# Optimization experiments

Measured on AMD Instinct MI355X. Metric: run time of the kernel, lower is better.

## Reference

```python
import jax, jax.numpy as jnp
import numpy as np

B, I, H = 16384, 1024, 1024
W_SCALE = 0.03  # keep gate pre-activations in a sane range (mimics small init)


def setup_inputs() -> dict:
    key = jax.random.key(0)
    ks = jax.random.split(key, 7)
    return {
        "x": jax.random.normal(ks[0], (B, I), dtype=jnp.float32),
        "c": jax.random.normal(ks[1], (B, H), dtype=jnp.float32),
        "h": jax.random.normal(ks[2], (B, H), dtype=jnp.float32),
        # gate order along axis 0: f (forget), i (input), k (cell cand), o (output)
        "Wx": jax.random.normal(ks[3], (4, H, I), dtype=jnp.float32) * W_SCALE,
        "bx": jax.random.normal(ks[4], (4, H), dtype=jnp.float32) * W_SCALE,
        "Wh": jax.random.normal(ks[5], (4, H, H), dtype=jnp.float32) * W_SCALE,
        "bh": jax.random.normal(ks[6], (4, H), dtype=jnp.float32) * W_SCALE,
    }


def reference(x, c, h, Wx, bx, Wh, bh):
    # Fused equivalent of the 8 tiny nn.Linear calls: one stacked GEMM each
    # for input->hidden and hidden->hidden. pre: [B, 4, H]
    pre = (jnp.einsum('bi,ghi->bgh', x, Wx)
           + jnp.einsum('bk,ghk->bgh', h, Wh)
           + bx[None] + bh[None])
    f = jax.nn.sigmoid(pre[:, 0])   # forget gate (w1/r1)
    i = jax.nn.sigmoid(pre[:, 1])   # input gate  (w2/r2)
    k = jnp.tanh(pre[:, 2])         # cell candidate (w3/r3)
    o = jax.nn.sigmoid(pre[:, 3])   # output gate (w4/r4)
    c_new = f * c + i * k
    h_new = o * jnp.tanh(c_new)
    return (o, c_new, h_new)
```

## Files before the change

kernel.cpp:

```cpp
#include <hip/hip_runtime.h>
#include <hip/hip_bf16.h>
#include <cstdint>

#define DI __device__ __forceinline__

typedef __attribute__((ext_vector_type(4)))  float f32x4;
typedef __attribute__((ext_vector_type(16))) float f32x16;
typedef __attribute__((ext_vector_type(8)))  short bf16x8;

static constexpr int B_ = 16384, I_ = 1024, H_ = 1024;
static constexpr int M = B_;
static constexpr int N = 4 * H_;
static constexpr int K = I_ + H_;
static constexpr int NT = K / 64;

static constexpr size_t OFF_A  = 0;
static constexpr size_t OFF_W  = OFF_A + (size_t)M * K * 2;
static constexpr size_t OFF_BI = OFF_W + (size_t)N * K * 2;

DI unsigned short f2bf(float f) {
    union { float f; unsigned u; } v; v.f = f;
    unsigned r = v.u + 0x7FFFu + ((v.u >> 16) & 1u);
    return (unsigned short)(r >> 16);
}

__global__ void cvt_kernel(const float* __restrict__ x, const float* __restrict__ h,
                           const float* __restrict__ Wx, const float* __restrict__ Wh,
                           unsigned short* __restrict__ A, unsigned short* __restrict__ W)
{
    long tid = (long)blockIdx.x * blockDim.x + threadIdx.x;
    long row = tid >> 9;
    int  col = (int)(tid & 511) * 4;
    const float* src;
    unsigned short* dst;
    if (row < M) {
        src = (col < I_) ? x + (size_t)row * I_ + col
                         : h + (size_t)row * H_ + (col - I_);
        dst = A + (size_t)row * K + col;
    } else {
        int r = (int)(row - M);
        int gate = (r >> 5) & 3;
        int hcol = ((r >> 7) << 5) | (r & 31);
        int srow = gate * H_ + hcol;
        src = (col < I_) ? Wx + (size_t)srow * I_ + col
                         : Wh + (size_t)srow * H_ + (col - I_);
        dst = W + (size_t)r * K + col;
    }
    float4 v = *(const float4*)src;
    ushort4 o;
    o.x = f2bf(v.x); o.y = f2bf(v.y); o.z = f2bf(v.z); o.w = f2bf(v.w);
    *(ushort4*)dst = o;
}

__global__ void bias_kernel(const float* __restrict__ bx, const float* __restrict__ bh,
                            float* __restrict__ bias)
{
    int r = blockIdx.x * blockDim.x + threadIdx.x;
    if (r < N) {
        int gate = (r >> 5) & 3;
        int hcol = ((r >> 7) << 5) | (r & 31);
        int s = gate * H_ + hcol;
        bias[r] = bx[s] + bh[s];
    }
}

DI void stage_half(const unsigned short* __restrict__ g, int grow0, int kcol,
                   unsigned short* ldsbase, int tid)
{
    const int w    = tid >> 6, lane = tid & 63;
    const int rsub = (w << 3) + (lane >> 3);
    const int kk   = kcol + (((lane & 7) ^ (lane >> 3)) << 3);
#pragma unroll
    for (int l = 0; l < 2; ++l) {
        const unsigned short* gp = g + (size_t)(grow0 + (l << 6) + rsub) * K + kk;
        unsigned short* lp = ldsbase + (((l << 6) + (w << 3)) << 6);
        __builtin_amdgcn_global_load_lds(
            (const __attribute__((address_space(1))) void*)gp,
            (__attribute__((address_space(3))) void*)lp, 16, 0, 0);
    }
}

DI bf16x8 ldfrag32(const unsigned short* tile, int row, int s16, int lane)
{
    const int sl = (((s16 << 1) + (lane >> 5)) ^ (row & 7));
    return *(const bf16x8*)(tile + (row << 6) + (sl << 3));
}

DI float sigf(float v) { return 1.f / (1.f + __expf(-v)); }
DI float tanhfast(float v) {
    float vc = fminf(fmaxf(v, -15.f), 15.f);
    float e  = __expf(2.f * vc);
    return (e - 1.f) / (e + 1.f);
}

__global__ __launch_bounds__(512, 2) void gemm_lstm(
    const unsigned short* __restrict__ Abf, const unsigned short* __restrict__ Wbf,
    const float* __restrict__ bias, const float* __restrict__ c,
    float* __restrict__ out)
{
    __shared__ __align__(16) unsigned short sh[65536];

    const int tid  = threadIdx.x;
    const int lane = tid & 63;
    const int wid  = tid >> 6;
    const int wr   = wid >> 1;
    const int wc   = wid & 1;

    const int bid  = blockIdx.x;
    const int xcd  = bid & 7;
    const int loc  = bid >> 3;
    const int nbk  = (xcd << 1) | (loc & 1);
    const int mbk  = loc >> 1;
    const int brow = mbk << 8, bcol = nbk << 8;

    const int l31  = lane & 31;
    const int rA0  = (wr << 6) + l31;
    const int rB0  = (wc << 7) + l31;

    f32x16 acc[2][4];
#pragma unroll
    for (int i = 0; i < 2; ++i)
#pragma unroll
        for (int j = 0; j < 4; ++j)
#pragma unroll
            for (int e = 0; e < 16; ++e) acc[i][j][e] = 0.f;
    bf16x8 a[4], b[4][4];

    {
        stage_half(Abf, brow,       0, sh,         tid);
        stage_half(Abf, brow + 128, 0, sh + 8192,  tid);
        stage_half(Wbf, bcol,       0, sh + 16384, tid);
        stage_half(Wbf, bcol + 128, 0, sh + 24576, tid);
        asm volatile("s_waitcnt vmcnt(0)" ::: "memory");
        __builtin_amdgcn_s_barrier();
    }

    for (int t = 0; t < NT; ++t) {
        const int q = t & 1;
        unsigned short* curA = sh + q * 32768;
        unsigned short* curB = curA + 16384;
        unsigned short* nxtA = sh + (q ^ 1) * 32768;
        unsigned short* nxtB = nxtA + 16384;
        const int k1 = ((t + 1) & 31) << 6;

        stage_half(Abf, brow,       k1, nxtA,        tid);
        stage_half(Abf, brow + 128, k1, nxtA + 8192, tid);
        stage_half(Wbf, bcol,       k1, nxtB,        tid);
        stage_half(Wbf, bcol + 128, k1, nxtB + 8192, tid);

#pragma unroll
        for (int nt = 0; nt < 4; ++nt)
#pragma unroll
            for (int s = 0; s < 4; ++s)
                b[nt][s] = ldfrag32(curB, rB0 + nt * 32, s, lane);

#pragma unroll
        for (int s = 0; s < 4; ++s) a[s] = ldfrag32(curA, rA0, s, lane);
#pragma unroll
        for (int s = 0; s < 4; ++s)
#pragma unroll
            for (int nt = 0; nt < 4; ++nt)
                acc[0][nt] = __builtin_amdgcn_mfma_f32_32x32x16_bf16(
                    a[s], b[nt][s], acc[0][nt], 0, 0, 0);

#pragma unroll
        for (int s = 0; s < 4; ++s) a[s] = ldfrag32(curA, rA0 + 32, s, lane);
#pragma unroll
        for (int s = 0; s < 4; ++s)
#pragma unroll
            for (int nt = 0; nt < 4; ++nt)
                acc[1][nt] = __builtin_amdgcn_mfma_f32_32x32x16_bf16(
                    a[s], b[nt][s], acc[1][nt], 0, 0, 0);

        asm volatile("s_waitcnt vmcnt(0)" ::: "memory");
        __builtin_amdgcn_s_barrier();
    }

    const int c0    = bcol + (wc << 7);
    const int hcol  = ((c0 >> 7) << 5) + l31;
    const float bs0 = bias[c0 +       l31];
    const float bs1 = bias[c0 +  32 + l31];
    const float bs2 = bias[c0 +  64 + l31];
    const float bs3 = bias[c0 +  96 + l31];
    const int rbase = brow + (wr << 6) + ((lane >> 5) << 2);
    const size_t P  = (size_t)B_ * H_;
#pragma unroll
    for (int mt = 0; mt < 2; ++mt) {
#pragma unroll
        for (int r = 0; r < 16; ++r) {
            const int row = rbase + mt * 32 + (r & 3) + ((r >> 2) << 3);
            const size_t base = (size_t)row * H_ + hcol;
            float fg = sigf(acc[mt][0][r] + bs0);
            float ig = sigf(acc[mt][1][r] + bs1);
            float kg = tanhfast(acc[mt][2][r] + bs2);
            float og = sigf(acc[mt][3][r] + bs3);
            float cv = c[base];
            float cn = fg * cv + ig * kg;
            float hn = og * tanhfast(cn);
            out[base]         = og;
            out[P + base]     = cn;
            out[2 * P + base] = hn;
        }
    }
}

extern "C" void kernel_launch(void* const* d_in, const int* in_sizes, int n_in,
                              void* d_out, int out_size, void* d_ws, size_t ws_size,
                              hipStream_t stream)
{
    const float* x  = (const float*)d_in[0];
    const float* c  = (const float*)d_in[1];
    const float* h  = (const float*)d_in[2];
    const float* Wx = (const float*)d_in[3];
    const float* bx = (const float*)d_in[4];
    const float* Wh = (const float*)d_in[5];
    const float* bh = (const float*)d_in[6];

    unsigned short* Abf  = (unsigned short*)((char*)d_ws + OFF_A);
    unsigned short* Wbf  = (unsigned short*)((char*)d_ws + OFF_W);
    float*          bias = (float*)((char*)d_ws + OFF_BI);
    float*          out  = (float*)d_out;

    cvt_kernel<<<40960, 256, 0, stream>>>(x, h, Wx, Wh, Abf, Wbf);
    bias_kernel<<<16, 256, 0, stream>>>(bx, bh, bias);
    gemm_lstm<<<(M / 256) * (N / 256), 512, 0, stream>>>(
        Abf, Wbf, bias, c, out);
}
```

Before: 350.6 us.

## Stage GEMM tiles in fragment-major LDS layout for conflict-free MFMA loads

Replaces the row-major, XOR-swizzled LDS tile layout with a fragment-major layout. Each wave loads 32 rows times 16 k-elements per global_load_lds, so every MFMA operand fragment sits contiguously in LDS and is read with a plain lane-indexed 16-byte load, with no swizzle arithmetic. It also loads both A fragments up front and interleaves the MFMAs across both M tiles, which raises register use. The intent is to cut LDS bank conflicts and address math in the inner loop. The cost is global loads where each lane fetches only 16 bytes from a different row, which may coalesce worse.

```diff
diff --git a/kernel.cpp b/kernel.cpp
--- a/kernel.cpp
+++ b/kernel.cpp
@@ -4,7 +4,6 @@
 
 #define DI __device__ __forceinline__
 
-typedef __attribute__((ext_vector_type(4)))  float f32x4;
 typedef __attribute__((ext_vector_type(16))) float f32x16;
 typedef __attribute__((ext_vector_type(8)))  short bf16x8;
 
@@ -64,26 +63,12 @@
     }
 }
 
-DI void stage_half(const unsigned short* __restrict__ g, int grow0, int kcol,
-                   unsigned short* ldsbase, int tid)
-{
-    const int w    = tid >> 6, lane = tid & 63;
-    const int rsub = (w << 3) + (lane >> 3);
-    const int kk   = kcol + (((lane & 7) ^ (lane >> 3)) << 3);
-#pragma unroll
-    for (int l = 0; l < 2; ++l) {
-        const unsigned short* gp = g + (size_t)(grow0 + (l << 6) + rsub) * K + kk;
-        unsigned short* lp = ldsbase + (((l << 6) + (w << 3)) << 6);
-        __builtin_amdgcn_global_load_lds(
-            (const __attribute__((address_space(1))) void*)gp,
-            (__attribute__((address_space(3))) void*)lp, 16, 0, 0);
-    }
-}
-
-DI bf16x8 ldfrag32(const unsigned short* tile, int row, int s16, int lane)
-{
-    const int sl = (((s16 << 1) + (lane >> 5)) ^ (row & 7));
-    return *(const bf16x8*)(tile + (row << 6) + (sl << 3));
+DI void stage_frag(const unsigned short* __restrict__ g, int srow, int kbase,
+                   unsigned short* lds)
+{
+    __builtin_amdgcn_global_load_lds(
+        (const __attribute__((address_space(1))) void*)(g + (size_t)srow * K + kbase),
+        (__attribute__((address_space(3))) void*)lds, 16, 0, 0);
 }
 
 DI float sigf(float v) { return 1.f / (1.f + __expf(-v)); }
@@ -114,8 +99,14 @@
     const int brow = mbk << 8, bcol = nbk << 8;
 
     const int l31  = lane & 31;
-    const int rA0  = (wr << 6) + l31;
-    const int rB0  = (wc << 7) + l31;
+    const int skoff = (lane >> 5) << 3;
+    const int srowA = brow + (wid << 5) + l31;
+    const int srowB = bcol + (wid << 5) + l31;
+    unsigned short* const ldsA = sh + ((wid << 2) << 9);
+    unsigned short* const ldsB = sh + 16384 + ((wid << 2) << 9);
+
+    const int faA = ((wr << 1) << 2);
+    const int faB = ((wc << 2) << 2);
 
     f32x16 acc[2][4];
 #pragma unroll
@@ -124,53 +115,52 @@
         for (int j = 0; j < 4; ++j)
 #pragma unroll
             for (int e = 0; e < 16; ++e) acc[i][j][e] = 0.f;
-    bf16x8 a[4], b[4][4];
+    bf16x8 a[2][4], b[4][4];
 
     {
-        stage_half(Abf, brow,       0, sh,         tid);
-        stage_half(Abf, brow + 128, 0, sh + 8192,  tid);
-        stage_half(Wbf, bcol,       0, sh + 16384, tid);
-        stage_half(Wbf, bcol + 128, 0, sh + 24576, tid);
+#pragma unroll
+        for (int i = 0; i < 4; ++i) {
+            stage_frag(Abf, srowA, (i << 4) + skoff, ldsA + (i << 9));
+            stage_frag(Wbf, srowB, (i << 4) + skoff, ldsB + (i << 9));
+        }
         asm volatile("s_waitcnt vmcnt(0)" ::: "memory");
         __builtin_amdgcn_s_barrier();
     }
 
     for (int t = 0; t < NT; ++t) {
         const int q = t & 1;
-        unsigned short* curA = sh + q * 32768;
+        unsigned short* curA = sh + (q << 15);
         unsigned short* curB = curA + 16384;
-        unsigned short* nxtA = sh + (q ^ 1) * 32768;
-        unsigned short* nxtB = nxtA + 16384;
+        const int nq = (q ^ 1) << 15;
         const int k1 = ((t + 1) & 31) << 6;
 
-        stage_half(Abf, brow,       k1, nxtA,        tid);
-        stage_half(Abf, brow + 128, k1, nxtA + 8192, tid);
-        stage_half(Wbf, bcol,       k1, nxtB,        tid);
-        stage_half(Wbf, bcol + 128, k1, nxtB + 8192, tid);
-
-#pragma unroll
-        for (int nt = 0; nt < 4; ++nt)
+#pragma unroll
+        for (int i = 0; i < 4; ++i) {
+            stage_frag(Abf, srowA, k1 + (i << 4) + skoff, ldsA + nq + (i << 9));
+            stage_frag(Wbf, srowB, k1 + (i << 4) + skoff, ldsB + nq + (i << 9));
+        }
+
+#pragma unroll
+        for (int nl = 0; nl < 4; ++nl)
 #pragma unroll
             for (int s = 0; s < 4; ++s)
-                b[nt][s] = ldfrag32(curB, rB0 + nt * 32, s, lane);
-
-#pragma unroll
-        for (int s = 0; s < 4; ++s) a[s] = ldfrag32(curA, rA0, s, lane);
+                b[nl][s] = *(const bf16x8*)(curB + (((faB + (nl << 2) + s) << 9))
+                                                 + (lane << 3));
+#pragma unroll
+        for (int ml = 0; ml < 2; ++ml)
+#pragma unroll
+            for (int s = 0; s < 4; ++s)
+                a[ml][s] = *(const bf16x8*)(curA + (((faA + (ml << 2) + s) << 9))
+                                                 + (lane << 3));
+
 #pragma unroll
         for (int s = 0; s < 4; ++s)
 #pragma unroll
-            for (int nt = 0; nt < 4; ++nt)
-                acc[0][nt] = __builtin_amdgcn_mfma_f32_32x32x16_bf16(
-                    a[s], b[nt][s], acc[0][nt], 0, 0, 0);
-
-#pragma unroll
-        for (int s = 0; s < 4; ++s) a[s] = ldfrag32(curA, rA0 + 32, s, lane);
-#pragma unroll
-        for (int s = 0; s < 4; ++s)
-#pragma unroll
-            for (int nt = 0; nt < 4; ++nt)
-                acc[1][nt] = __builtin_amdgcn_mfma_f32_32x32x16_bf16(
-                    a[s], b[nt][s], acc[1][nt], 0, 0, 0);
+            for (int ml = 0; ml < 2; ++ml)
+#pragma unroll
+                for (int nl = 0; nl < 4; ++nl)
+                    acc[ml][nl] = __builtin_amdgcn_mfma_f32_32x32x16_bf16(
+                        a[ml][s], b[nl][s], acc[ml][nl], 0, 0, 0);
 
         asm volatile("s_waitcnt vmcnt(0)" ::: "memory");
         __builtin_amdgcn_s_barrier();
```

Measured after the change: 453.1 us. 29.2% more time.
